# Kernel tuning notes

Hardware: AMD Instinct MI355X
Metric: run time of the kernel (lower is better)

The kernel has to match this reference:

```python
import jax, jax.numpy as jnp
import numpy as np

BOND_D = 4    # disentangler bond dim (hard-coded 4 in torch init)
BOND_I = 16   # isometry bond dim (bond_dim kwarg)
F = 2         # feature_dim = 2*nCh, nCh=1 -> [x, 1-x] embedding
LEVELS = [128, 64, 32, 16, 8, 4]
NUM_CLASSES = 10
BATCH = 16


def setup_inputs() -> dict:
    key = jax.random.key(0)
    ks = iter(jax.random.split(key, 128))
    inp = {}
    inp["x"] = jax.random.uniform(next(ks), (BATCH, 1, 128, 128), dtype=jnp.float32)

    def mps_params(P, D, O):
        A = 0.2 * jax.random.normal(next(ks), (P, 4, F, D, D), dtype=jnp.float32)
        v = 0.2 * jax.random.normal(next(ks), (P, D), dtype=jnp.float32)
        w = 0.2 * jax.random.normal(next(ks), (P, D, O), dtype=jnp.float32)
        return A, v, w

    for l, H in enumerate(LEVELS, start=1):
        Pd = ((H - 2) // 2) ** 2   # number of disentangler patches
        Pi = (H // 2) ** 2         # number of isometry patches
        inp[f"d{l}A"], inp[f"d{l}v"], inp[f"d{l}w"] = mps_params(Pd, BOND_D, 4)
        inp[f"i{l}A"], inp[f"i{l}v"], inp[f"i{l}w"] = mps_params(Pi, BOND_I, 1)
    inp["fA"], inp["fv"], inp["fw"] = mps_params(1, BOND_I, NUM_CLASSES)
    return inp


def _patches(x):
    # x: [b, H, W] (H, W even) -> [b, (H/2)*(W/2), 4], same site order as
    # torch unfold(2,2,2).unfold(3,2,2).reshape(..., 4)
    b, H, W = x.shape
    return x.reshape(b, H // 2, 2, W // 2, 2).transpose(0, 1, 3, 2, 4).reshape(b, -1, 4)


def _unpatch(y, nh, nw):
    # y: [b, nh*nw, 4] -> [b, 2*nh, 2*nw], inverse spatial placement of 2x2 blocks
    b = y.shape[0]
    return y.reshape(b, nh, nw, 2, 2).transpose(0, 1, 3, 2, 4).reshape(b, 2 * nh, 2 * nw)


def _mps(patches, A, v, w):
    # Batched per-patch ReLU-MPS over 4 sites.
    # patches [b,P,4], A [P,4,F,D,D], v [P,D], w [P,D,O] -> [b,P,O]
    phi = jnp.stack([patches, 1.0 - patches], axis=-1)          # [b,P,4,F]
    M = jnp.einsum('bpsf,psfij->bpsij', phi, A)                 # [b,P,4,D,D]
    vec = jnp.einsum('pi,bpij->bpj', v, M[:, :, 0])             # [b,P,D]
    for s in range(1, 4):
        vec = jnp.einsum('bpi,bpij->bpj', vec, M[:, :, s])
    return jax.nn.relu(jnp.einsum('bpi,pio->bpo', vec, w))


def _level(x, dA, dv, dw, iA, iv, iw):
    # One MERA layer: disentangle shifted interior patches, write back, then
    # isometry-pool the full grid 2x2 -> 1.
    b, H, W = x.shape
    nh = (H - 2) // 2
    y = _mps(_patches(x[:, 1:-1, 1:-1]), dA, dv, dw)            # [b, nh*nh, 4]
    x = x.at[:, 1:-1, 1:-1].set(_unpatch(y, nh, nh))
    y2 = _mps(_patches(x), iA, iv, iw)                          # [b, (H/2)^2, 1]
    return y2.reshape(b, H // 2, W // 2)


def reference(x, d1A, d1v, d1w, i1A, i1v, i1w,
              d2A, d2v, d2w, i2A, i2v, i2w,
              d3A, d3v, d3w, i3A, i3v, i3w,
              d4A, d4v, d4w, i4A, i4v, i4w,
              d5A, d5v, d5w, i5A, i5v, i5w,
              d6A, d6v, d6w, i6A, i6v, i6w,
              fA, fv, fw):
    h = x[:, 0]  # nCh = 1
    levels = [(d1A, d1v, d1w, i1A, i1v, i1w), (d2A, d2v, d2w, i2A, i2v, i2w),
              (d3A, d3v, d3w, i3A, i3v, i3w), (d4A, d4v, d4w, i4A, i4v, i4w),
              (d5A, d5v, d5w, i5A, i5v, i5w), (d6A, d6v, d6w, i6A, i6v, i6w)]
    for p in levels:
        h = _level(h, *p)
    flat = h.reshape(h.shape[0], 1, 4)         # final 2x2 grid -> 4 sites
    return _mps(flat, fA, fv, fw)[:, 0]        # [b, NUM_CLASSES]
```

## Files before the change

kernel.cpp:

```cpp
#include <hip/hip_runtime.h>

#define BATCH 16

template <int H>
__device__ __forceinline__ float fused_di_unit(
    const float* __restrict__ xb, int p, int j,
    const float* __restrict__ dA, const float* __restrict__ dv,
    const float* __restrict__ dw,
    const float* __restrict__ iA, const float* __restrict__ iv,
    const float* __restrict__ iw) {
  constexpr int NH = (H - 2) / 2;
  constexpr int W2 = H / 2;
  int pi = p / W2, pj = p % W2;
  int sg = j >> 2, j4 = j & 3;
  int r = 2 * pi + (sg >> 1), c = 2 * pj + (sg & 1);
  float tcell;
  bool border = (r == 0) | (r == H - 1) | (c == 0) | (c == H - 1);
  if (border) {
    tcell = xb[r * H + c];
  } else {
    int dpi = (r - 1) >> 1, dpj = (c - 1) >> 1;
    int sd = ((r - 1) & 1) * 2 + ((c - 1) & 1);
    int dp = dpi * NH + dpj;
    int R0 = 1 + 2 * dpi, C0 = 1 + 2 * dpj;
    float tin = xb[(R0 + (j4 >> 1)) * H + (C0 + (j4 & 1))];
    const float* Ap = dA + dp * 128;
    float vec = dv[dp * 4 + j4];
#pragma unroll
    for (int s = 0; s < 4; s++) {
      float ts = __shfl(tin, s, 4);
      const float* A0 = Ap + s * 32;
      float q0 = 0.f, q1 = 0.f;
#pragma unroll
      for (int i = 0; i < 4; i++) {
        float sv = __shfl(vec, i, 4);
        q0 = fmaf(sv, A0[i * 4 + j4], q0);
        q1 = fmaf(sv, A0[16 + i * 4 + j4], q1);
      }
      vec = ts * q0 + (1.0f - ts) * q1;
    }
    float y = 0.f;
#pragma unroll
    for (int i = 0; i < 4; i++)
      y = fmaf(__shfl(vec, i, 4), dw[dp * 16 + i * 4 + j4], y);
    y = fmaxf(y, 0.0f);
    tcell = __shfl(y, sd, 4);
  }
  float t[4];
  t[0] = __shfl(tcell, 0, 16);
  t[1] = __shfl(tcell, 4, 16);
  t[2] = __shfl(tcell, 8, 16);
  t[3] = __shfl(tcell, 12, 16);
  const float* Ap = iA + p * 2048;
  float vec = iv[p * 16 + j];
#pragma unroll
  for (int s = 0; s < 4; s++) {
    const float* A0 = Ap + s * 512;
    float q0 = 0.f, q1 = 0.f;
#pragma unroll
    for (int i = 0; i < 16; i++) {
      float sv = __shfl(vec, i, 16);
      q0 = fmaf(sv, A0[i * 16 + j], q0);
      q1 = fmaf(sv, A0[256 + i * 16 + j], q1);
    }
    vec = t[s] * q0 + (1.0f - t[s]) * q1;
  }
  float partial = vec * iw[p * 16 + j];
#pragma unroll
  for (int off = 8; off >= 1; off >>= 1)
    partial += __shfl_xor(partial, off, 16);
  return fmaxf(partial, 0.0f);
}

template <int H>
__global__ __launch_bounds__(256) void level_kernel(
    const float* __restrict__ xin, float* __restrict__ hn,
    const float* __restrict__ dA, const float* __restrict__ dv,
    const float* __restrict__ dw, const float* __restrict__ iA,
    const float* __restrict__ iv, const float* __restrict__ iw) {
  constexpr int W2 = H / 2;
  int g = blockIdx.x * 256 + threadIdx.x;
  int j = g & 15;
  int b = (g >> 4) & 15;
  int p = g >> 8;
  const float* xb = xin + b * H * H;
  float o = fused_di_unit<H>(xb, p, j, dA, dv, dw, iA, iv, iw);
  if (j == 0) hn[b * W2 * W2 + p] = o;
}

struct Tail2Args {
  const float* h4;
  const float* in[15];
  float* out;
};

__global__ __launch_bounds__(256) void tail2_kernel(Tail2Args a) {
  __shared__ float x5[64];
  __shared__ float h5[16];
  __shared__ float h6[4];
  int b = blockIdx.x;
  int tid = threadIdx.x;
  if (tid < 64) x5[tid] = a.h4[b * 64 + tid];
  __syncthreads();
  {
    int j = tid & 15, p = tid >> 4;
    float o = fused_di_unit<8>(x5, p, j, a.in[0], a.in[1], a.in[2],
                               a.in[3], a.in[4], a.in[5]);
    if (j == 0) h5[p] = o;
  }
  __syncthreads();
  if (tid < 64) {
    int j = tid & 15, p = tid >> 4;
    float o = fused_di_unit<4>(h5, p, j, a.in[6], a.in[7], a.in[8],
                               a.in[9], a.in[10], a.in[11]);
    if (j == 0) h6[p] = o;
  }
  __syncthreads();
  if (tid < 16) {
    int j = tid;
    const float* fA = a.in[12];
    const float* fv = a.in[13];
    const float* fw = a.in[14];
    float t[4] = {h6[0], h6[1], h6[2], h6[3]};
    float vec = fv[j];
#pragma unroll
    for (int s = 0; s < 4; s++) {
      const float* A0 = fA + s * 512;
      float q0 = 0.f, q1 = 0.f;
#pragma unroll
      for (int i = 0; i < 16; i++) {
        float sv = __shfl(vec, i, 16);
        q0 = fmaf(sv, A0[i * 16 + j], q0);
        q1 = fmaf(sv, A0[256 + i * 16 + j], q1);
      }
      vec = t[s] * q0 + (1.0f - t[s]) * q1;
    }
    float acc = 0.0f;
#pragma unroll
    for (int i = 0; i < 16; i++) {
      float sv = __shfl(vec, i, 16);
      float wv = (j < 10) ? fw[i * 10 + j] : 0.0f;
      acc = fmaf(sv, wv, acc);
    }
    if (j < 10) a.out[b * 10 + j] = fmaxf(acc, 0.0f);
  }
}

extern "C" void kernel_launch(void* const* d_in, const int* in_sizes, int n_in,
                              void* d_out, int out_size, void* d_ws, size_t ws_size,
                              hipStream_t stream) {
  const float* x = (const float*)d_in[0];
  float* ws = (float*)d_ws;
  float* h1 = ws;
  float* h2 = h1 + 65536;
  float* h3 = h2 + 16384;
  float* h4 = h3 + 4096;

  level_kernel<128><<<4096, 256, 0, stream>>>(
      x, h1, (const float*)d_in[1], (const float*)d_in[2],
      (const float*)d_in[3], (const float*)d_in[4], (const float*)d_in[5],
      (const float*)d_in[6]);
  level_kernel<64><<<1024, 256, 0, stream>>>(
      h1, h2, (const float*)d_in[7], (const float*)d_in[8],
      (const float*)d_in[9], (const float*)d_in[10], (const float*)d_in[11],
      (const float*)d_in[12]);
  level_kernel<32><<<256, 256, 0, stream>>>(
      h2, h3, (const float*)d_in[13], (const float*)d_in[14],
      (const float*)d_in[15], (const float*)d_in[16], (const float*)d_in[17],
      (const float*)d_in[18]);
  level_kernel<16><<<64, 256, 0, stream>>>(
      h3, h4, (const float*)d_in[19], (const float*)d_in[20],
      (const float*)d_in[21], (const float*)d_in[22], (const float*)d_in[23],
      (const float*)d_in[24]);

  Tail2Args ta;
  ta.h4 = h4;
  for (int i = 0; i < 15; i++) ta.in[i] = (const float*)d_in[25 + i];
  ta.out = (float*)d_out;
  tail2_kernel<<<BATCH, 256, 0, stream>>>(ta);
}
```

Before: 212.0 us.

## Use 4 lanes per MPS with float4 loads, DPP permutes, batch-interleaved layout

Each isometry MPS now runs on 4 lanes that each own 4 bond components, instead of 16 lanes with one component each. Parameters are read as float4 and broadcasts go through DPP quad permutes rather than ds_bpermute shuffles. The disentangler chain runs entirely inside one lane, which drops its 4-lane shuffles. Intermediate grids are stored batch-interleaved ([p][b]) so that consecutive threads with the same patch share parameter loads. The level-16 kernel is folded into the tail kernel, removing one launch. Each thread now does more serial work and holds more registers, and the grids are smaller.

```diff
diff --git a/kernel.cpp b/kernel.cpp
--- a/kernel.cpp
+++ b/kernel.cpp
@@ -2,9 +2,50 @@
 
 #define BATCH 16
 
-template <int H>
-__device__ __forceinline__ float fused_di_unit(
-    const float* __restrict__ xb, int p, int j,
+template <int CTRL>
+__device__ __forceinline__ float qperm(float x) {
+  int xi = __float_as_int(x);
+  return __int_as_float(__builtin_amdgcn_update_dpp(xi, xi, CTRL, 0xF, 0xF, true));
+}
+
+__device__ __forceinline__ float4 f4fma(float s, float4 a, float4 c) {
+  c.x = fmaf(s, a.x, c.x);
+  c.y = fmaf(s, a.y, c.y);
+  c.z = fmaf(s, a.z, c.z);
+  c.w = fmaf(s, a.w, c.w);
+  return c;
+}
+
+__device__ __forceinline__ void mps16_chain(const float* __restrict__ A,
+                                            int jq, const float tt[4],
+                                            float vec[4]) {
+#pragma unroll
+  for (int s = 0; s < 4; s++) {
+    const float4* A0v = (const float4*)(A + s * 512) + jq;
+    const float4* A1v = A0v + 64;
+    float4 q0 = {0.f, 0.f, 0.f, 0.f}, q1 = {0.f, 0.f, 0.f, 0.f};
+#define ISTEP(i)                                         \
+  {                                                      \
+    float sv = qperm<(((i) >> 2) * 0x55)>(vec[(i) & 3]); \
+    q0 = f4fma(sv, A0v[(i) * 4], q0);                    \
+    q1 = f4fma(sv, A1v[(i) * 4], q1);                    \
+  }
+    ISTEP(0) ISTEP(1) ISTEP(2) ISTEP(3)
+    ISTEP(4) ISTEP(5) ISTEP(6) ISTEP(7)
+    ISTEP(8) ISTEP(9) ISTEP(10) ISTEP(11)
+    ISTEP(12) ISTEP(13) ISTEP(14) ISTEP(15)
+#undef ISTEP
+    float ph = tt[s], om = 1.0f - ph;
+    vec[0] = ph * q0.x + om * q1.x;
+    vec[1] = ph * q0.y + om * q1.y;
+    vec[2] = ph * q0.z + om * q1.z;
+    vec[3] = ph * q0.w + om * q1.w;
+  }
+}
+
+template <int H, int XS>
+__device__ __forceinline__ float fused_di_quad(
+    const float* __restrict__ xb, int p, int jq,
     const float* __restrict__ dA, const float* __restrict__ dv,
     const float* __restrict__ dw,
     const float* __restrict__ iA, const float* __restrict__ iv,
@@ -12,137 +53,144 @@
   constexpr int NH = (H - 2) / 2;
   constexpr int W2 = H / 2;
   int pi = p / W2, pj = p % W2;
-  int sg = j >> 2, j4 = j & 3;
-  int r = 2 * pi + (sg >> 1), c = 2 * pj + (sg & 1);
+  int r = 2 * pi + (jq >> 1), c = 2 * pj + (jq & 1);
   float tcell;
   bool border = (r == 0) | (r == H - 1) | (c == 0) | (c == H - 1);
   if (border) {
-    tcell = xb[r * H + c];
+    tcell = xb[(r * H + c) * XS];
   } else {
     int dpi = (r - 1) >> 1, dpj = (c - 1) >> 1;
     int sd = ((r - 1) & 1) * 2 + ((c - 1) & 1);
     int dp = dpi * NH + dpj;
     int R0 = 1 + 2 * dpi, C0 = 1 + 2 * dpj;
-    float tin = xb[(R0 + (j4 >> 1)) * H + (C0 + (j4 & 1))];
-    const float* Ap = dA + dp * 128;
-    float vec = dv[dp * 4 + j4];
+    float tins[4];
+    tins[0] = xb[(R0 * H + C0) * XS];
+    tins[1] = xb[(R0 * H + C0 + 1) * XS];
+    tins[2] = xb[((R0 + 1) * H + C0) * XS];
+    tins[3] = xb[((R0 + 1) * H + C0 + 1) * XS];
+    const float4* Av = (const float4*)(dA + dp * 128);
+    float4 dvv = *(const float4*)(dv + dp * 4);
+    float v0 = dvv.x, v1 = dvv.y, v2 = dvv.z, v3 = dvv.w;
 #pragma unroll
     for (int s = 0; s < 4; s++) {
-      float ts = __shfl(tin, s, 4);
-      const float* A0 = Ap + s * 32;
-      float q0 = 0.f, q1 = 0.f;
-#pragma unroll
-      for (int i = 0; i < 4; i++) {
-        float sv = __shfl(vec, i, 4);
-        q0 = fmaf(sv, A0[i * 4 + j4], q0);
-        q1 = fmaf(sv, A0[16 + i * 4 + j4], q1);
-      }
-      vec = ts * q0 + (1.0f - ts) * q1;
+      const float4* A0 = Av + s * 8;
+      float4 q0 = {0.f, 0.f, 0.f, 0.f}, q1 = {0.f, 0.f, 0.f, 0.f};
+      q0 = f4fma(v0, A0[0], q0);
+      q0 = f4fma(v1, A0[1], q0);
+      q0 = f4fma(v2, A0[2], q0);
+      q0 = f4fma(v3, A0[3], q0);
+      q1 = f4fma(v0, A0[4], q1);
+      q1 = f4fma(v1, A0[5], q1);
+      q1 = f4fma(v2, A0[6], q1);
+      q1 = f4fma(v3, A0[7], q1);
+      float ph = tins[s], om = 1.0f - ph;
+      v0 = ph * q0.x + om * q1.x;
+      v1 = ph * q0.y + om * q1.y;
+      v2 = ph * q0.z + om * q1.z;
+      v3 = ph * q0.w + om * q1.w;
     }
-    float y = 0.f;
-#pragma unroll
-    for (int i = 0; i < 4; i++)
-      y = fmaf(__shfl(vec, i, 4), dw[dp * 16 + i * 4 + j4], y);
-    y = fmaxf(y, 0.0f);
-    tcell = __shfl(y, sd, 4);
-  }
-  float t[4];
-  t[0] = __shfl(tcell, 0, 16);
-  t[1] = __shfl(tcell, 4, 16);
-  t[2] = __shfl(tcell, 8, 16);
-  t[3] = __shfl(tcell, 12, 16);
-  const float* Ap = iA + p * 2048;
-  float vec = iv[p * 16 + j];
-#pragma unroll
-  for (int s = 0; s < 4; s++) {
-    const float* A0 = Ap + s * 512;
-    float q0 = 0.f, q1 = 0.f;
-#pragma unroll
-    for (int i = 0; i < 16; i++) {
-      float sv = __shfl(vec, i, 16);
-      q0 = fmaf(sv, A0[i * 16 + j], q0);
-      q1 = fmaf(sv, A0[256 + i * 16 + j], q1);
-    }
-    vec = t[s] * q0 + (1.0f - t[s]) * q1;
-  }
-  float partial = vec * iw[p * 16 + j];
-#pragma unroll
-  for (int off = 8; off >= 1; off >>= 1)
-    partial += __shfl_xor(partial, off, 16);
+    const float* wp = dw + dp * 16 + sd;
+    float y = v0 * wp[0];
+    y = fmaf(v1, wp[4], y);
+    y = fmaf(v2, wp[8], y);
+    y = fmaf(v3, wp[12], y);
+    tcell = fmaxf(y, 0.0f);
+  }
+  float tt[4];
+  tt[0] = qperm<0x00>(tcell);
+  tt[1] = qperm<0x55>(tcell);
+  tt[2] = qperm<0xAA>(tcell);
+  tt[3] = qperm<0xFF>(tcell);
+  float4 vv = *(const float4*)(iv + p * 16 + 4 * jq);
+  float vec[4] = {vv.x, vv.y, vv.z, vv.w};
+  mps16_chain(iA + (size_t)p * 2048, jq, tt, vec);
+  float4 wv = *(const float4*)(iw + p * 16 + 4 * jq);
+  float partial = vec[0] * wv.x;
+  partial = fmaf(vec[1], wv.y, partial);
+  partial = fmaf(vec[2], wv.z, partial);
+  partial = fmaf(vec[3], wv.w, partial);
+  partial += qperm<0xB1>(partial);
+  partial += qperm<0x4E>(partial);
   return fmaxf(partial, 0.0f);
 }
 
-template <int H>
+template <int H, int BP, int XS>
 __global__ __launch_bounds__(256) void level_kernel(
     const float* __restrict__ xin, float* __restrict__ hn,
     const float* __restrict__ dA, const float* __restrict__ dv,
     const float* __restrict__ dw, const float* __restrict__ iA,
     const float* __restrict__ iv, const float* __restrict__ iw) {
-  constexpr int W2 = H / 2;
-  int g = blockIdx.x * 256 + threadIdx.x;
-  int j = g & 15;
-  int b = (g >> 4) & 15;
-  int p = g >> 8;
-  const float* xb = xin + b * H * H;
-  float o = fused_di_unit<H>(xb, p, j, dA, dv, dw, iA, iv, iw);
-  if (j == 0) hn[b * W2 * W2 + p] = o;
-}
-
-struct Tail2Args {
-  const float* h4;
-  const float* in[15];
+  int tid = threadIdx.x;
+  int jq = tid & 3;
+  int b = (tid >> 2) & 15;
+  int p = blockIdx.x * BP + (tid >> 6);
+  const float* xb = (XS == 1) ? (xin + b * H * H) : (xin + b);
+  float o = fused_di_quad<H, XS>(xb, p, jq, dA, dv, dw, iA, iv, iw);
+  if (jq == 0) hn[p * 16 + b] = o;
+}
+
+struct TailArgs {
+  const float* h3;
+  const float* in[21];
   float* out;
 };
 
-__global__ __launch_bounds__(256) void tail2_kernel(Tail2Args a) {
+__global__ __launch_bounds__(256) void tail_kernel(TailArgs a) {
+  __shared__ float x4[256];
   __shared__ float x5[64];
-  __shared__ float h5[16];
+  __shared__ float x6[16];
   __shared__ float h6[4];
   int b = blockIdx.x;
   int tid = threadIdx.x;
-  if (tid < 64) x5[tid] = a.h4[b * 64 + tid];
+  x4[tid] = a.h3[tid * 16 + b];
   __syncthreads();
   {
-    int j = tid & 15, p = tid >> 4;
-    float o = fused_di_unit<8>(x5, p, j, a.in[0], a.in[1], a.in[2],
-                               a.in[3], a.in[4], a.in[5]);
-    if (j == 0) h5[p] = o;
+    int jq = tid & 3, p = tid >> 2;
+    float o = fused_di_quad<16, 1>(x4, p, jq, a.in[0], a.in[1], a.in[2],
+                                   a.in[3], a.in[4], a.in[5]);
+    if (jq == 0) x5[p] = o;
   }
   __syncthreads();
   if (tid < 64) {
-    int j = tid & 15, p = tid >> 4;
-    float o = fused_di_unit<4>(h5, p, j, a.in[6], a.in[7], a.in[8],
-                               a.in[9], a.in[10], a.in[11]);
-    if (j == 0) h6[p] = o;
+    int jq = tid & 3, p = tid >> 2;
+    float o = fused_di_quad<8, 1>(x5, p, jq, a.in[6], a.in[7], a.in[8],
+                                  a.in[9], a.in[10], a.in[11]);
+    if (jq == 0) x6[p] = o;
   }
   __syncthreads();
   if (tid < 16) {
-    int j = tid;
-    const float* fA = a.in[12];
-    const float* fv = a.in[13];
-    const float* fw = a.in[14];
-    float t[4] = {h6[0], h6[1], h6[2], h6[3]};
-    float vec = fv[j];
-#pragma unroll
-    for (int s = 0; s < 4; s++) {
-      const float* A0 = fA + s * 512;
-      float q0 = 0.f, q1 = 0.f;
-#pragma unroll
-      for (int i = 0; i < 16; i++) {
-        float sv = __shfl(vec, i, 16);
-        q0 = fmaf(sv, A0[i * 16 + j], q0);
-        q1 = fmaf(sv, A0[256 + i * 16 + j], q1);
-      }
-      vec = t[s] * q0 + (1.0f - t[s]) * q1;
+    int jq = tid & 3, p = tid >> 2;
+    float o = fused_di_quad<4, 1>(x6, p, jq, a.in[12], a.in[13], a.in[14],
+                                  a.in[15], a.in[16], a.in[17]);
+    if (jq == 0) h6[p] = o;
+  }
+  __syncthreads();
+  if (tid < 4) {
+    int jq = tid;
+    const float* fA = a.in[18];
+    const float* fv = a.in[19];
+    const float* fw = a.in[20];
+    float tt[4] = {h6[0], h6[1], h6[2], h6[3]};
+    float4 vv = *(const float4*)(fv + 4 * jq);
+    float vec[4] = {vv.x, vv.y, vv.z, vv.w};
+    mps16_chain(fA, jq, tt, vec);
+    float acc[10];
+#pragma unroll
+    for (int o = 0; o < 10; o++) acc[o] = 0.f;
+#pragma unroll
+    for (int k = 0; k < 4; k++)
+#pragma unroll
+      for (int o = 0; o < 10; o++)
+        acc[o] = fmaf(vec[k], fw[(4 * jq + k) * 10 + o], acc[o]);
+#pragma unroll
+    for (int o = 0; o < 10; o++) {
+      acc[o] += qperm<0xB1>(acc[o]);
+      acc[o] += qperm<0x4E>(acc[o]);
     }
-    float acc = 0.0f;
-#pragma unroll
-    for (int i = 0; i < 16; i++) {
-      float sv = __shfl(vec, i, 16);
-      float wv = (j < 10) ? fw[i * 10 + j] : 0.0f;
-      acc = fmaf(sv, wv, acc);
+    if (jq == 0) {
+#pragma unroll
+      for (int o = 0; o < 10; o++) a.out[b * 10 + o] = fmaxf(acc[o], 0.0f);
     }
-    if (j < 10) a.out[b * 10 + j] = fmaxf(acc, 0.0f);
   }
 }
 
@@ -154,28 +202,23 @@
   float* h1 = ws;
   float* h2 = h1 + 65536;
   float* h3 = h2 + 16384;
-  float* h4 = h3 + 4096;
-
-  level_kernel<128><<<4096, 256, 0, stream>>>(
+
+  level_kernel<128, 4, 1><<<1024, 256, 0, stream>>>(
       x, h1, (const float*)d_in[1], (const float*)d_in[2],
       (const float*)d_in[3], (const float*)d_in[4], (const float*)d_in[5],
       (const float*)d_in[6]);
-  level_kernel<64><<<1024, 256, 0, stream>>>(
+  level_kernel<64, 4, 16><<<256, 256, 0, stream>>>(
       h1, h2, (const float*)d_in[7], (const float*)d_in[8],
       (const float*)d_in[9], (const float*)d_in[10], (const float*)d_in[11],
       (const float*)d_in[12]);
-  level_kernel<32><<<256, 256, 0, stream>>>(
+  level_kernel<32, 1, 16><<<256, 64, 0, stream>>>(
       h2, h3, (const float*)d_in[13], (const float*)d_in[14],
       (const float*)d_in[15], (const float*)d_in[16], (const float*)d_in[17],
       (const float*)d_in[18]);
-  level_kernel<16><<<64, 256, 0, stream>>>(
-      h3, h4, (const float*)d_in[19], (const float*)d_in[20],
-      (const float*)d_in[21], (const float*)d_in[22], (const float*)d_in[23],
-      (const float*)d_in[24]);
-
-  Tail2Args ta;
-  ta.h4 = h4;
-  for (int i = 0; i < 15; i++) ta.in[i] = (const float*)d_in[25 + i];
+
+  TailArgs ta;
+  ta.h3 = h3;
+  for (int i = 0; i < 21; i++) ta.in[i] = (const float*)d_in[19 + i];
   ta.out = (float*)d_out;
-  tail2_kernel<<<BATCH, 256, 0, stream>>>(ta);
-}
+  tail_kernel<<<BATCH, 256, 0, stream>>>(ta);
+}
```

Result: slower. 222.7 us (+5.0%).
